# Kernel optimization log

Measured on AMD Instinct MI355X. Metric: run time of the kernel, lower is better.

Reference implementation:

```python
import jax, jax.numpy as jnp
import numpy as np

SIGMA = 0.1

def setup_inputs() -> dict:
    key = jax.random.key(0)
    k1, k2, k3 = jax.random.split(key, 3)
    B, BANDS, P, K = 128, 256, 32, 64
    x = jax.random.normal(k1, (B, 1, BANDS, P, P), dtype=jnp.float32)
    mu = 0.001 * jax.random.normal(k2, (BANDS,), dtype=jnp.float32)
    noise = jax.random.normal(k3, (BANDS,), dtype=jnp.float32)
    extra_noise = jnp.zeros((BANDS,), dtype=jnp.float32)
    return {"x": x, "mu": mu, "noise": noise, "extra_noise": extra_noise, "k": K}


def reference(x, mu, noise, extra_noise, k):
    # stochastic gate: z = mu + sigma*(noise + 0.25*extra_noise) (training=True, discount=1)
    z = mu + SIGMA * (noise + 0.25 * extra_noise)
    gate = jnp.clip(z + 0.5, 0.0, 1.0)  # hard_sigmoid, [bands]

    xs = x[:, 0]  # squeeze -> [B, bands, P, P]
    # stable top-k: with no ties this equals sorted top-k indices
    _, idx = jax.lax.top_k(gate, k)
    idx = jnp.sort(idx)  # [k]

    xg = xs[:, idx]  # gather bands -> [B, k, P, P]
    # transpose(1,3) * gate[topk] * transpose(1,3) == broadcast over band axis
    out = xg * gate[idx][None, :, None, None]
    return out[:, None]  # unsqueeze(1) -> [B, 1, k, P, P]
```

## Files before the change

### kernel.cpp

```cpp
#include <hip/hip_runtime.h>

#define SIGMA 0.1f
#define BANDS 256
#define KSEL  64

__global__ void FeatureSelector_topk(const float* __restrict__ mu,
                                     const float* __restrict__ noise,
                                     const float* __restrict__ extra,
                                     int*   __restrict__ ws_idx,
                                     float* __restrict__ ws_gate) {
    __shared__ float g[BANDS];
    __shared__ unsigned long long masks[BANDS / 64];
    const int tid  = threadIdx.x;
    const int wave = tid >> 6;
    const int lane = tid & 63;

    float z = mu[tid] + SIGMA * (noise[tid] + 0.25f * extra[tid]) + 0.5f;
    float gate = fminf(fmaxf(z, 0.0f), 1.0f);
    g[tid] = gate;
    __syncthreads();

    int rank = 0;
#pragma unroll 8
    for (int j = 0; j < BANDS; ++j) {
        float gj = g[j];
        rank += (gj > gate) || (gj == gate && j < tid);
    }
    const bool sel = rank < KSEL;

    unsigned long long m = __ballot(sel);
    if (lane == 0) masks[wave] = m;
    __syncthreads();

    if (sel) {
        int pos = __popcll(m & ((1ull << lane) - 1ull));
        for (int w = 0; w < wave; ++w) pos += __popcll(masks[w]);
        ws_idx[pos]  = tid;
        ws_gate[pos] = gate;
    }
}

__global__ void FeatureSelector_gather(const float4* __restrict__ x,
                                       const int*    __restrict__ ws_idx,
                                       const float*  __restrict__ ws_gate,
                                       float4*       __restrict__ out) {
    const int pair = blockIdx.x;
    const int bj0  = pair << 1;
    const int b    = bj0 >> 6;
    const int j0   = bj0 & (KSEL - 1);
    const int tid  = threadIdx.x;

    const int   band0 = ws_idx[j0];
    const int   band1 = ws_idx[j0 + 1];
    const float s0    = ws_gate[j0];
    const float s1    = ws_gate[j0 + 1];

    float4 v0 = x[(b * BANDS + band0) * 256 + tid];
    float4 v1 = x[(b * BANDS + band1) * 256 + tid];
    v0.x *= s0; v0.y *= s0; v0.z *= s0; v0.w *= s0;
    v1.x *= s1; v1.y *= s1; v1.z *= s1; v1.w *= s1;
    out[(b * KSEL + j0) * 256 + tid]     = v0;
    out[(b * KSEL + j0 + 1) * 256 + tid] = v1;
}

extern "C" void kernel_launch(void* const* d_in, const int* in_sizes, int n_in,
                              void* d_out, int out_size, void* d_ws, size_t ws_size,
                              hipStream_t stream) {
    const float* x     = (const float*)d_in[0];
    const float* mu    = (const float*)d_in[1];
    const float* noise = (const float*)d_in[2];
    const float* extra = (const float*)d_in[3];

    int*   ws_idx  = (int*)d_ws;
    float* ws_gate = (float*)((char*)d_ws + KSEL * sizeof(int));

    FeatureSelector_topk<<<1, BANDS, 0, stream>>>(mu, noise, extra, ws_idx, ws_gate);

    const int B = 128;
    FeatureSelector_gather<<<(B * KSEL) / 2, 256, 0, stream>>>(
        (const float4*)x, ws_idx, ws_gate, (float4*)d_out);
}
```

Measured before the change: 193.7 us.

## Fuse top-k selection into gather kernel, recomputing per block with four planes

Merges the single-block top-k kernel and the gather kernel into one launch. Each block now recomputes the gate and rank-based top-k selection in LDS, then gathers and scales four band planes instead of two. This removes a kernel launch and the dependency gap between the two kernels. In exchange every block repeats a 256x256 comparison loop, and the grid is halved, so there is more memory-level parallelism per thread but fewer blocks.

```diff
diff --git a/kernel.cpp b/kernel.cpp
--- a/kernel.cpp
+++ b/kernel.cpp
@@ -3,14 +3,19 @@
 #define SIGMA 0.1f
 #define BANDS 256
 #define KSEL  64
+#define PPB   4
 
-__global__ void FeatureSelector_topk(const float* __restrict__ mu,
-                                     const float* __restrict__ noise,
-                                     const float* __restrict__ extra,
-                                     int*   __restrict__ ws_idx,
-                                     float* __restrict__ ws_gate) {
+__global__ void __launch_bounds__(BANDS)
+FeatureSelector_fused(const float4* __restrict__ x,
+                      const float*  __restrict__ mu,
+                      const float*  __restrict__ noise,
+                      const float*  __restrict__ extra,
+                      float4*       __restrict__ out) {
     __shared__ float g[BANDS];
     __shared__ unsigned long long masks[BANDS / 64];
+    __shared__ int   lds_idx[KSEL];
+    __shared__ float lds_gate[KSEL];
+
     const int tid  = threadIdx.x;
     const int wave = tid >> 6;
     const int lane = tid & 63;
@@ -21,7 +26,7 @@
     __syncthreads();
 
     int rank = 0;
-#pragma unroll 8
+#pragma unroll 16
     for (int j = 0; j < BANDS; ++j) {
         float gj = g[j];
         rank += (gj > gate) || (gj == gate && j < tid);
@@ -35,32 +40,32 @@
     if (sel) {
         int pos = __popcll(m & ((1ull << lane) - 1ull));
         for (int w = 0; w < wave; ++w) pos += __popcll(masks[w]);
-        ws_idx[pos]  = tid;
-        ws_gate[pos] = gate;
+        lds_idx[pos]  = tid;
+        lds_gate[pos] = gate;
     }
-}
+    __syncthreads();
 
-__global__ void FeatureSelector_gather(const float4* __restrict__ x,
-                                       const int*    __restrict__ ws_idx,
-                                       const float*  __restrict__ ws_gate,
-                                       float4*       __restrict__ out) {
-    const int pair = blockIdx.x;
-    const int bj0  = pair << 1;
-    const int b    = bj0 >> 6;
-    const int j0   = bj0 & (KSEL - 1);
-    const int tid  = threadIdx.x;
+    const int bj0 = blockIdx.x * PPB;
+    const int b   = bj0 >> 6;
+    const int j0  = bj0 & (KSEL - 1);
 
-    const int   band0 = ws_idx[j0];
-    const int   band1 = ws_idx[j0 + 1];
-    const float s0    = ws_gate[j0];
-    const float s1    = ws_gate[j0 + 1];
+    int   band[PPB];
+    float s[PPB];
+#pragma unroll
+    for (int p = 0; p < PPB; ++p) {
+        band[p] = lds_idx[j0 + p];
+        s[p]    = lds_gate[j0 + p];
+    }
 
-    float4 v0 = x[(b * BANDS + band0) * 256 + tid];
-    float4 v1 = x[(b * BANDS + band1) * 256 + tid];
-    v0.x *= s0; v0.y *= s0; v0.z *= s0; v0.w *= s0;
-    v1.x *= s1; v1.y *= s1; v1.z *= s1; v1.w *= s1;
-    out[(b * KSEL + j0) * 256 + tid]     = v0;
-    out[(b * KSEL + j0 + 1) * 256 + tid] = v1;
+    float4 v[PPB];
+#pragma unroll
+    for (int p = 0; p < PPB; ++p)
+        v[p] = x[(b * BANDS + band[p]) * 256 + tid];
+#pragma unroll
+    for (int p = 0; p < PPB; ++p) {
+        v[p].x *= s[p]; v[p].y *= s[p]; v[p].z *= s[p]; v[p].w *= s[p];
+        out[(b * KSEL + j0 + p) * 256 + tid] = v[p];
+    }
 }
 
 extern "C" void kernel_launch(void* const* d_in, const int* in_sizes, int n_in,
@@ -71,12 +76,7 @@
     const float* noise = (const float*)d_in[2];
     const float* extra = (const float*)d_in[3];
 
-    int*   ws_idx  = (int*)d_ws;
-    float* ws_gate = (float*)((char*)d_ws + KSEL * sizeof(int));
-
-    FeatureSelector_topk<<<1, BANDS, 0, stream>>>(mu, noise, extra, ws_idx, ws_gate);
-
     const int B = 128;
-    FeatureSelector_gather<<<(B * KSEL) / 2, 256, 0, stream>>>(
-        (const float4*)x, ws_idx, ws_gate, (float4*)d_out);
+    FeatureSelector_fused<<<(B * KSEL) / PPB, BANDS, 0, stream>>>(
+        (const float4*)x, mu, noise, extra, (float4*)d_out);
 }
```

Result: slower. 199.6 us (+3.1%).
